# Kernel optimization log

Hardware: AMD Instinct MI355X
Metric: run time of the kernel (lower is better)

## Reference

```python
import jax, jax.numpy as jnp
import numpy as np

EPS = 1e-05
IN_FEATURES = 1024
OUT_FEATURES = 512
M = 65536


def setup_inputs() -> dict:
    key = jax.random.key(0)
    k_x, k_w, k_b = jax.random.split(key, 3)
    x = jax.random.normal(k_x, (M, IN_FEATURES), dtype=jnp.float32)
    # kaiming_uniform(a=sqrt(5)) on [out, in]: bound = sqrt(6/((1+a^2)*fan_in)) = 1/sqrt(fan_in)
    bound = 1.0 / np.sqrt(IN_FEATURES)
    weight = jax.random.uniform(k_w, (OUT_FEATURES, IN_FEATURES), dtype=jnp.float32,
                                minval=-bound, maxval=bound)
    bias = jax.random.uniform(k_b, (OUT_FEATURES,), dtype=jnp.float32,
                              minval=-bound, maxval=bound)
    gamma = jnp.ones((OUT_FEATURES,), dtype=jnp.float32)
    beta = jnp.zeros((OUT_FEATURES,), dtype=jnp.float32)
    scale = jnp.ones((1,), dtype=jnp.float32)
    return {"x": x, "weight": weight, "bias": bias,
            "gamma": gamma, "beta": beta, "scale": scale}


def reference(x, weight, bias, gamma, beta, scale):
    # GEMM + bias: [M, N]
    acc = jnp.einsum('mk,nk->mn', x, weight) + bias[None, :]
    # Row-wise normalization over N (as the fused kernel computes per row)
    mean = jnp.mean(acc, axis=1, keepdims=True)
    var = jnp.mean((acc - mean) ** 2, axis=1, keepdims=True)
    normalized = (acc - mean) / jnp.sqrt(var + EPS)
    scaled = (normalized * gamma[None, :] + beta[None, :]) * scale[0]
    # Row softmax over N
    return jax.nn.softmax(scaled, axis=1)
```

## Files before the change

### kernel.cpp

```cpp
#include <hip/hip_runtime.h>
#include <hip/hip_bf16.h>

constexpr int KD = 1024;
constexpr int ND = 512;
constexpr int NT = 16;
constexpr float EPSV = 1e-5f;

using f32x4  = __attribute__((ext_vector_type(4))) float;
using bf16x8 = __attribute__((ext_vector_type(8))) short;
using u16x8  = __attribute__((ext_vector_type(8))) unsigned short;

__device__ __forceinline__ unsigned short f2bf(float f) {
  unsigned int u = __builtin_bit_cast(unsigned int, f);
  return (unsigned short)((u + 0x7fffu + ((u >> 16) & 1u)) >> 16);
}

__device__ __forceinline__ u16x8 pack8(float4 a, float4 b) {
  u16x8 v;
  v[0] = f2bf(a.x); v[1] = f2bf(a.y); v[2] = f2bf(a.z); v[3] = f2bf(a.w);
  v[4] = f2bf(b.x); v[5] = f2bf(b.y); v[6] = f2bf(b.z); v[7] = f2bf(b.w);
  return v;
}

__device__ __forceinline__ unsigned short cvt1(float f) {
  __hip_bfloat16 h = __float2bfloat16(f);
  return __builtin_bit_cast(unsigned short, h);
}

__device__ __forceinline__ float bf2f(unsigned short s) {
  unsigned int u = (unsigned int)s << 16;
  return __builtin_bit_cast(float, u);
}

__device__ __forceinline__ void gload16(const void* g, void* l) {
  __builtin_amdgcn_global_load_lds(
      (const __attribute__((address_space(1))) void*)g,
      (__attribute__((address_space(3))) void*)l, 16, 0, 0);
}

#define WAITV8()  asm volatile("s_waitcnt vmcnt(8)" ::: "memory")
#define WAITV0()  asm volatile("s_waitcnt vmcnt(0)" ::: "memory")
#define LGKM0()   do { asm volatile("s_waitcnt lgkmcnt(0)" ::: "memory"); \
                       __builtin_amdgcn_sched_barrier(0); } while (0)
#define SCHEDB()  __builtin_amdgcn_sched_barrier(0)

__global__ void wconvert_kernel(const float* __restrict__ w,
                                unsigned short* __restrict__ wb) {
  int i = (blockIdx.x * blockDim.x + threadIdx.x) * 8;
  float4 a = *reinterpret_cast<const float4*>(w + i);
  float4 b = *reinterpret_cast<const float4*>(w + i + 4);
  *reinterpret_cast<u16x8*>(wb + i) = pack8(a, b);
}

__global__ __launch_bounds__(512, 2)
void fused_kernel(const float* __restrict__ x,
                  const unsigned short* __restrict__ wb,
                  const float* __restrict__ bias,
                  const float* __restrict__ gamma,
                  const float* __restrict__ beta,
                  const float* __restrict__ scalep,
                  float* __restrict__ out) {
  __shared__ unsigned short As[2][128 * 64];
  __shared__ unsigned short Bs[2][512 * 64];

  const int tid  = threadIdx.x;
  const int lane = tid & 63;
  const int wid  = tid >> 6;
  const int wr   = wid >> 2;
  const int wcq  = wid & 3;
  const int l15  = lane & 15;
  const int lg   = lane >> 4;

  const long bm  = (long)blockIdx.x * 128;

  f32x4 acc[4][8] = {};

  const int arow0 = wid * 16 + lg;
  const float* asrc = x + (bm + arow0) * KD + l15 * 4;
  int aw[4];
  #pragma unroll
  for (int q = 0; q < 4; ++q) {
    int row = arow0 + q * 4;
    aw[q] = row * 128 + (((l15 >> 1) ^ (row & 7)) * 16) + ((l15 & 1) * 8);
  }

  int bsrc[8];
  #pragma unroll
  for (int p = 0; p < 8; ++p) {
    int n = p * 64 + (tid >> 3);
    int u = (tid & 7) ^ (n & 7);
    bsrc[p] = n * KD + u * 8;
  }

  int ard[4], brd[8];
  #pragma unroll
  for (int i = 0; i < 4; ++i) {
    int row = wr * 64 + i * 16 + l15;
    ard[i] = row * 128 + (lg ^ (row & 7)) * 16;
  }
  #pragma unroll
  for (int i = 0; i < 8; ++i) {
    int n = wcq * 128 + i * 16 + l15;
    brd[i] = n * 128 + (lg ^ (n & 7)) * 16;
  }

#define ISSUE_A(t) do { \
    qa0 = *reinterpret_cast<const float4*>(asrc + (t) * 64 + 0 * 4 * KD); \
    qa1 = *reinterpret_cast<const float4*>(asrc + (t) * 64 + 1 * 4 * KD); \
    qa2 = *reinterpret_cast<const float4*>(asrc + (t) * 64 + 2 * 4 * KD); \
    qa3 = *reinterpret_cast<const float4*>(asrc + (t) * 64 + 3 * 4 * KD); } while (0)

#define ISSUE_B(t, bufi) do { \
    gload16(wb + bsrc[0] + (t) * 64, (char*)Bs[bufi] + 0 * 8192 + tid * 16); \
    gload16(wb + bsrc[1] + (t) * 64, (char*)Bs[bufi] + 1 * 8192 + tid * 16); \
    gload16(wb + bsrc[2] + (t) * 64, (char*)Bs[bufi] + 2 * 8192 + tid * 16); \
    gload16(wb + bsrc[3] + (t) * 64, (char*)Bs[bufi] + 3 * 8192 + tid * 16); \
    gload16(wb + bsrc[4] + (t) * 64, (char*)Bs[bufi] + 4 * 8192 + tid * 16); \
    gload16(wb + bsrc[5] + (t) * 64, (char*)Bs[bufi] + 5 * 8192 + tid * 16); \
    gload16(wb + bsrc[6] + (t) * 64, (char*)Bs[bufi] + 6 * 8192 + tid * 16); \
    gload16(wb + bsrc[7] + (t) * 64, (char*)Bs[bufi] + 7 * 8192 + tid * 16); } while (0)

#define WA1(qr, qi, bufi) do { \
    union { unsigned short s[4]; unsigned long long v; } c_; \
    c_.s[0] = cvt1(qr.x); c_.s[1] = cvt1(qr.y); \
    c_.s[2] = cvt1(qr.z); c_.s[3] = cvt1(qr.w); \
    *reinterpret_cast<unsigned long long*>((char*)As[bufi] + aw[qi]) = c_.v; } while (0)

#define WRITE_A(bufi) do { const int wb_ = (bufi); \
    WA1(qa0, 0, wb_); WA1(qa1, 1, wb_); WA1(qa2, 2, wb_); WA1(qa3, 3, wb_); } while (0)

#define PHASE(ks, bufc) do { \
    const char* ab_ = (const char*)As[bufc]; \
    const char* bb_ = (const char*)Bs[bufc]; \
    const int kx_ = (ks) * 64; \
    bf16x8 b0_ = *reinterpret_cast<const bf16x8*>(bb_ + (brd[0] ^ kx_)); \
    bf16x8 b1_ = *reinterpret_cast<const bf16x8*>(bb_ + (brd[1] ^ kx_)); \
    bf16x8 b2_ = *reinterpret_cast<const bf16x8*>(bb_ + (brd[2] ^ kx_)); \
    bf16x8 b3_ = *reinterpret_cast<const bf16x8*>(bb_ + (brd[3] ^ kx_)); \
    bf16x8 b4_ = *reinterpret_cast<const bf16x8*>(bb_ + (brd[4] ^ kx_)); \
    bf16x8 b5_ = *reinterpret_cast<const bf16x8*>(bb_ + (brd[5] ^ kx_)); \
    bf16x8 b6_ = *reinterpret_cast<const bf16x8*>(bb_ + (brd[6] ^ kx_)); \
    bf16x8 b7_ = *reinterpret_cast<const bf16x8*>(bb_ + (brd[7] ^ kx_)); \
    bf16x8 a0_ = *reinterpret_cast<const bf16x8*>(ab_ + (ard[0] ^ kx_)); \
    bf16x8 a1_ = *reinterpret_cast<const bf16x8*>(ab_ + (ard[1] ^ kx_)); \
    bf16x8 a2_ = *reinterpret_cast<const bf16x8*>(ab_ + (ard[2] ^ kx_)); \
    bf16x8 a3_ = *reinterpret_cast<const bf16x8*>(ab_ + (ard[3] ^ kx_)); \
    LGKM0(); \
    __builtin_amdgcn_s_setprio(1); \
    acc[0][0] = __builtin_amdgcn_mfma_f32_16x16x32_bf16(a0_, b0_, acc[0][0], 0, 0, 0); \
    acc[0][1] = __builtin_amdgcn_mfma_f32_16x16x32_bf16(a0_, b1_, acc[0][1], 0, 0, 0); \
    acc[0][2] = __builtin_amdgcn_mfma_f32_16x16x32_bf16(a0_, b2_, acc[0][2], 0, 0, 0); \
    acc[0][3] = __builtin_amdgcn_mfma_f32_16x16x32_bf16(a0_, b3_, acc[0][3], 0, 0, 0); \
    acc[0][4] = __builtin_amdgcn_mfma_f32_16x16x32_bf16(a0_, b4_, acc[0][4], 0, 0, 0); \
    acc[0][5] = __builtin_amdgcn_mfma_f32_16x16x32_bf16(a0_, b5_, acc[0][5], 0, 0, 0); \
    acc[0][6] = __builtin_amdgcn_mfma_f32_16x16x32_bf16(a0_, b6_, acc[0][6], 0, 0, 0); \
    acc[0][7] = __builtin_amdgcn_mfma_f32_16x16x32_bf16(a0_, b7_, acc[0][7], 0, 0, 0); \
    acc[1][0] = __builtin_amdgcn_mfma_f32_16x16x32_bf16(a1_, b0_, acc[1][0], 0, 0, 0); \
    acc[1][1] = __builtin_amdgcn_mfma_f32_16x16x32_bf16(a1_, b1_, acc[1][1], 0, 0, 0); \
    acc[1][2] = __builtin_amdgcn_mfma_f32_16x16x32_bf16(a1_, b2_, acc[1][2], 0, 0, 0); \
    acc[1][3] = __builtin_amdgcn_mfma_f32_16x16x32_bf16(a1_, b3_, acc[1][3], 0, 0, 0); \
    acc[1][4] = __builtin_amdgcn_mfma_f32_16x16x32_bf16(a1_, b4_, acc[1][4], 0, 0, 0); \
    acc[1][5] = __builtin_amdgcn_mfma_f32_16x16x32_bf16(a1_, b5_, acc[1][5], 0, 0, 0); \
    acc[1][6] = __builtin_amdgcn_mfma_f32_16x16x32_bf16(a1_, b6_, acc[1][6], 0, 0, 0); \
    acc[1][7] = __builtin_amdgcn_mfma_f32_16x16x32_bf16(a1_, b7_, acc[1][7], 0, 0, 0); \
    acc[2][0] = __builtin_amdgcn_mfma_f32_16x16x32_bf16(a2_, b0_, acc[2][0], 0, 0, 0); \
    acc[2][1] = __builtin_amdgcn_mfma_f32_16x16x32_bf16(a2_, b1_, acc[2][1], 0, 0, 0); \
    acc[2][2] = __builtin_amdgcn_mfma_f32_16x16x32_bf16(a2_, b2_, acc[2][2], 0, 0, 0); \
    acc[2][3] = __builtin_amdgcn_mfma_f32_16x16x32_bf16(a2_, b3_, acc[2][3], 0, 0, 0); \
    acc[2][4] = __builtin_amdgcn_mfma_f32_16x16x32_bf16(a2_, b4_, acc[2][4], 0, 0, 0); \
    acc[2][5] = __builtin_amdgcn_mfma_f32_16x16x32_bf16(a2_, b5_, acc[2][5], 0, 0, 0); \
    acc[2][6] = __builtin_amdgcn_mfma_f32_16x16x32_bf16(a2_, b6_, acc[2][6], 0, 0, 0); \
    acc[2][7] = __builtin_amdgcn_mfma_f32_16x16x32_bf16(a2_, b7_, acc[2][7], 0, 0, 0); \
    acc[3][0] = __builtin_amdgcn_mfma_f32_16x16x32_bf16(a3_, b0_, acc[3][0], 0, 0, 0); \
    acc[3][1] = __builtin_amdgcn_mfma_f32_16x16x32_bf16(a3_, b1_, acc[3][1], 0, 0, 0); \
    acc[3][2] = __builtin_amdgcn_mfma_f32_16x16x32_bf16(a3_, b2_, acc[3][2], 0, 0, 0); \
    acc[3][3] = __builtin_amdgcn_mfma_f32_16x16x32_bf16(a3_, b3_, acc[3][3], 0, 0, 0); \
    acc[3][4] = __builtin_amdgcn_mfma_f32_16x16x32_bf16(a3_, b4_, acc[3][4], 0, 0, 0); \
    acc[3][5] = __builtin_amdgcn_mfma_f32_16x16x32_bf16(a3_, b5_, acc[3][5], 0, 0, 0); \
    acc[3][6] = __builtin_amdgcn_mfma_f32_16x16x32_bf16(a3_, b6_, acc[3][6], 0, 0, 0); \
    acc[3][7] = __builtin_amdgcn_mfma_f32_16x16x32_bf16(a3_, b7_, acc[3][7], 0, 0, 0); \
    __builtin_amdgcn_s_setprio(0); \
    SCHEDB(); } while (0)

  float4 qa0, qa1, qa2, qa3;

  ISSUE_A(0);    SCHEDB();
  ISSUE_B(0, 0); SCHEDB();
  WAITV8();
  WRITE_A(0);
  WAITV0();
  LGKM0();
  __builtin_amdgcn_s_barrier();
  SCHEDB();

  for (int t = 0; t < NT; ++t) {
    const int cur = t & 1;
    const int tp  = (t + 1 < NT) ? t + 1 : NT - 1;
    ISSUE_A(tp);          SCHEDB();
    PHASE(0, cur);
    ISSUE_B(tp, cur ^ 1); SCHEDB();
    PHASE(1, cur);
    WAITV8();
    WRITE_A(cur ^ 1);
    WAITV0();
    LGKM0();
    __builtin_amdgcn_s_barrier();
    SCHEDB();
  }

  float* redS = (float*)As[0];
  float* redQ = redS + 640;
  float* rowA = redQ + 640;
  float* rowB = rowA + 128;

  const int col0 = wcq * 128 + l15;
  const float sc = scalep[0];
  float bs8[8], gs8[8], bb8[8];
  #pragma unroll
  for (int ni = 0; ni < 8; ++ni) {
    bs8[ni] = bias[col0 + ni * 16];
    gs8[ni] = gamma[col0 + ni * 16] * sc;
    bb8[ni] = beta[col0 + ni * 16] * sc;
  }

  #pragma unroll
  for (int mi = 0; mi < 4; ++mi) {
    #pragma unroll
    for (int j = 0; j < 4; ++j) {
      float s = 0.f, q = 0.f;
      #pragma unroll
      for (int ni = 0; ni < 8; ++ni) {
        float v = acc[mi][ni][j] + bs8[ni];
        acc[mi][ni][j] = v;
        s += v;
        q = fmaf(v, v, q);
      }
      #pragma unroll
      for (int m = 1; m < 16; m <<= 1) {
        s += __shfl_xor(s, m, 64);
        q += __shfl_xor(q, m, 64);
      }
      if (l15 == 0) {
        int r = wr * 64 + mi * 16 + lg * 4 + j;
        redS[r * 5 + wcq] = s;
        redQ[r * 5 + wcq] = q;
      }
    }
  }
  __syncthreads();
  if (tid < 128) {
    float s = redS[tid * 5 + 0] + redS[tid * 5 + 1] + redS[tid * 5 + 2] + redS[tid * 5 + 3];
    float q = redQ[tid * 5 + 0] + redQ[tid * 5 + 1] + redQ[tid * 5 + 2] + redQ[tid * 5 + 3];
    float mu = s * (1.f / ND);
    rowA[tid] = mu;
    rowB[tid] = rsqrtf(q * (1.f / ND) - mu * mu + EPSV);
  }
  __syncthreads();

  #pragma unroll
  for (int mi = 0; mi < 4; ++mi) {
    #pragma unroll
    for (int j = 0; j < 4; ++j) {
      int r = wr * 64 + mi * 16 + lg * 4 + j;
      float mu = rowA[r], rs = rowB[r];
      float pm = -3.402823466e38f;
      #pragma unroll
      for (int ni = 0; ni < 8; ++ni) {
        float v = (acc[mi][ni][j] - mu) * rs;
        v = fmaf(v, gs8[ni], bb8[ni]);
        acc[mi][ni][j] = v;
        pm = fmaxf(pm, v);
      }
      #pragma unroll
      for (int m = 1; m < 16; m <<= 1) pm = fmaxf(pm, __shfl_xor(pm, m, 64));
      if (l15 == 0) redS[r * 5 + wcq] = pm;
    }
  }
  __syncthreads();
  if (tid < 128) {
    rowA[tid] = fmaxf(fmaxf(redS[tid * 5 + 0], redS[tid * 5 + 1]),
                      fmaxf(redS[tid * 5 + 2], redS[tid * 5 + 3]));
  }
  __syncthreads();

  #pragma unroll
  for (int mi = 0; mi < 4; ++mi) {
    #pragma unroll
    for (int j = 0; j < 4; ++j) {
      int r = wr * 64 + mi * 16 + lg * 4 + j;
      float rmx = rowA[r];
      float ps = 0.f;
      #pragma unroll
      for (int ni = 0; ni < 8; ++ni) {
        float e = __expf(acc[mi][ni][j] - rmx);
        acc[mi][ni][j] = e;
        ps += e;
      }
      #pragma unroll
      for (int m = 1; m < 16; m <<= 1) ps += __shfl_xor(ps, m, 64);
      if (l15 == 0) redQ[r * 5 + wcq] = ps;
    }
  }
  __syncthreads();
  if (tid < 128) {
    rowB[tid] = 1.f / (redQ[tid * 5 + 0] + redQ[tid * 5 + 1] +
                       redQ[tid * 5 + 2] + redQ[tid * 5 + 3]);
  }
  __syncthreads();

  #pragma unroll
  for (int mi = 0; mi < 4; ++mi) {
    #pragma unroll
    for (int j = 0; j < 4; ++j) {
      int r = wr * 64 + mi * 16 + lg * 4 + j;
      float rd = rowB[r];
      float* op = out + (bm + r) * ND + col0;
      #pragma unroll
      for (int ni = 0; ni < 8; ++ni)
        __builtin_nontemporal_store(acc[mi][ni][j] * rd, op + ni * 16);
    }
  }
#undef ISSUE_A
#undef ISSUE_B
#undef WA1
#undef WRITE_A
#undef PHASE
}

__global__ void fused_fallback(const float* __restrict__ x,
                               const float* __restrict__ wf,
                               const float* __restrict__ bias,
                               const float* __restrict__ gamma,
                               const float* __restrict__ beta,
                               const float* __restrict__ scalep,
                               float* __restrict__ out) {
  long row = blockIdx.x;
  int t = threadIdx.x;
  float s = 0.f;
  const float* xr = x + row * KD;
  const float* wr_ = wf + (size_t)t * KD;
  for (int k = 0; k < KD; ++k) s += xr[k] * wr_[k];
  s += bias[t];
  __shared__ float buf[ND];
  buf[t] = s;
  __syncthreads();
  __shared__ float red[2];
  if (t == 0) {
    float sum = 0.f, sq = 0.f;
    for (int i = 0; i < ND; ++i) { sum += buf[i]; sq += buf[i] * buf[i]; }
    float mu = sum / ND;
    red[0] = mu;
    red[1] = rsqrtf(sq / ND - mu * mu + EPSV);
  }
  __syncthreads();
  float zv = (s - red[0]) * red[1] * gamma[t] * scalep[0] + beta[t] * scalep[0];
  buf[t] = zv;
  __syncthreads();
  __shared__ float red2[2];
  if (t == 0) {
    float mxv = -3.4e38f;
    for (int i = 0; i < ND; ++i) mxv = fmaxf(mxv, buf[i]);
    float den = 0.f;
    for (int i = 0; i < ND; ++i) den += __expf(buf[i] - mxv);
    red2[0] = mxv; red2[1] = 1.f / den;
  }
  __syncthreads();
  out[row * ND + t] = __expf(zv - red2[0]) * red2[1];
}

extern "C" void kernel_launch(void* const* d_in, const int* in_sizes, int n_in,
                              void* d_out, int out_size, void* d_ws, size_t ws_size,
                              hipStream_t stream) {
  const float* x     = (const float*)d_in[0];
  const float* w     = (const float*)d_in[1];
  const float* bias  = (const float*)d_in[2];
  const float* gamma = (const float*)d_in[3];
  const float* beta  = (const float*)d_in[4];
  const float* scale = (const float*)d_in[5];
  float* out = (float*)d_out;

  const int Mrows = in_sizes[0] / KD;
  const size_t wb_bytes = (size_t)ND * KD * sizeof(unsigned short);

  if (ws_size >= wb_bytes) {
    unsigned short* wbuf = (unsigned short*)d_ws;
    wconvert_kernel<<<(ND * KD) / (256 * 8), 256, 0, stream>>>(w, wbuf);
    fused_kernel<<<Mrows / 128, 512, 0, stream>>>(x, wbuf, bias, gamma, beta,
                                                  scale, out);
  } else {
    fused_fallback<<<Mrows, ND, 0, stream>>>(x, w, bias, gamma, beta, scale, out);
  }
}
```

Measured before the change: 140.5 us.

## Use 1024-thread blocks with 64-column wave tiles and earlier B prefetch

Doubles the block to 16 waves, each computing a 64x64 tile instead of 64x128, halving accumulator registers per thread and splitting A/B global loads across more threads. The B tile prefetch for the next k-step is issued before the first MFMA phase instead of between phases. Row reductions for layernorm and softmax now combine 8 per-wave partials. This adds more LDS fragment reads overall and a larger block that may limit scheduling flexibility.

Result: no change. 139.1 us (-0.9%).

```diff
diff --git a/kernel.cpp b/kernel.cpp
--- a/kernel.cpp
+++ b/kernel.cpp
@@ -27,18 +27,13 @@
   return __builtin_bit_cast(unsigned short, h);
 }
 
-__device__ __forceinline__ float bf2f(unsigned short s) {
-  unsigned int u = (unsigned int)s << 16;
-  return __builtin_bit_cast(float, u);
-}
-
 __device__ __forceinline__ void gload16(const void* g, void* l) {
   __builtin_amdgcn_global_load_lds(
       (const __attribute__((address_space(1))) void*)g,
       (__attribute__((address_space(3))) void*)l, 16, 0, 0);
 }
 
-#define WAITV8()  asm volatile("s_waitcnt vmcnt(8)" ::: "memory")
+#define WAITV4()  asm volatile("s_waitcnt vmcnt(4)" ::: "memory")
 #define WAITV0()  asm volatile("s_waitcnt vmcnt(0)" ::: "memory")
 #define LGKM0()   do { asm volatile("s_waitcnt lgkmcnt(0)" ::: "memory"); \
                        __builtin_amdgcn_sched_barrier(0); } while (0)
@@ -52,7 +47,7 @@
   *reinterpret_cast<u16x8*>(wb + i) = pack8(a, b);
 }
 
-__global__ __launch_bounds__(512, 2)
+__global__ __launch_bounds__(1024, 4)
 void fused_kernel(const float* __restrict__ x,
                   const unsigned short* __restrict__ wb,
                   const float* __restrict__ bias,
@@ -66,59 +61,53 @@
   const int tid  = threadIdx.x;
   const int lane = tid & 63;
   const int wid  = tid >> 6;
-  const int wr   = wid >> 2;
-  const int wcq  = wid & 3;
+  const int wr   = wid >> 3;
+  const int wcn  = wid & 7;
   const int l15  = lane & 15;
   const int lg   = lane >> 4;
 
   const long bm  = (long)blockIdx.x * 128;
 
-  f32x4 acc[4][8] = {};
-
-  const int arow0 = wid * 16 + lg;
+  f32x4 acc[4][4] = {};
+
+  const int arow0 = wid * 8 + lg;
   const float* asrc = x + (bm + arow0) * KD + l15 * 4;
-  int aw[4];
-  #pragma unroll
-  for (int q = 0; q < 4; ++q) {
+  int aw[2];
+  #pragma unroll
+  for (int q = 0; q < 2; ++q) {
     int row = arow0 + q * 4;
     aw[q] = row * 128 + (((l15 >> 1) ^ (row & 7)) * 16) + ((l15 & 1) * 8);
   }
 
-  int bsrc[8];
-  #pragma unroll
-  for (int p = 0; p < 8; ++p) {
-    int n = p * 64 + (tid >> 3);
+  int bsrc[4];
+  #pragma unroll
+  for (int p = 0; p < 4; ++p) {
+    int n = p * 128 + (tid >> 3);
     int u = (tid & 7) ^ (n & 7);
     bsrc[p] = n * KD + u * 8;
   }
 
-  int ard[4], brd[8];
+  int ard[4], brd[4];
   #pragma unroll
   for (int i = 0; i < 4; ++i) {
     int row = wr * 64 + i * 16 + l15;
     ard[i] = row * 128 + (lg ^ (row & 7)) * 16;
   }
   #pragma unroll
-  for (int i = 0; i < 8; ++i) {
-    int n = wcq * 128 + i * 16 + l15;
+  for (int i = 0; i < 4; ++i) {
+    int n = wcn * 64 + i * 16 + l15;
     brd[i] = n * 128 + (lg ^ (n & 7)) * 16;
   }
 
 #define ISSUE_A(t) do { \
     qa0 = *reinterpret_cast<const float4*>(asrc + (t) * 64 + 0 * 4 * KD); \
-    qa1 = *reinterpret_cast<const float4*>(asrc + (t) * 64 + 1 * 4 * KD); \
-    qa2 = *reinterpret_cast<const float4*>(asrc + (t) * 64 + 2 * 4 * KD); \
-    qa3 = *reinterpret_cast<const float4*>(asrc + (t) * 64 + 3 * 4 * KD); } while (0)
+    qa1 = *reinterpret_cast<const float4*>(asrc + (t) * 64 + 1 * 4 * KD); } while (0)
 
 #define ISSUE_B(t, bufi) do { \
-    gload16(wb + bsrc[0] + (t) * 64, (char*)Bs[bufi] + 0 * 8192 + tid * 16); \
-    gload16(wb + bsrc[1] + (t) * 64, (char*)Bs[bufi] + 1 * 8192 + tid * 16); \
-    gload16(wb + bsrc[2] + (t) * 64, (char*)Bs[bufi] + 2 * 8192 + tid * 16); \
-    gload16(wb + bsrc[3] + (t) * 64, (char*)Bs[bufi] + 3 * 8192 + tid * 16); \
-    gload16(wb + bsrc[4] + (t) * 64, (char*)Bs[bufi] + 4 * 8192 + tid * 16); \
-    gload16(wb + bsrc[5] + (t) * 64, (char*)Bs[bufi] + 5 * 8192 + tid * 16); \
-    gload16(wb + bsrc[6] + (t) * 64, (char*)Bs[bufi] + 6 * 8192 + tid * 16); \
-    gload16(wb + bsrc[7] + (t) * 64, (char*)Bs[bufi] + 7 * 8192 + tid * 16); } while (0)
+    gload16(wb + bsrc[0] + (t) * 64, (char*)Bs[bufi] + 0 * 16384 + tid * 16); \
+    gload16(wb + bsrc[1] + (t) * 64, (char*)Bs[bufi] + 1 * 16384 + tid * 16); \
+    gload16(wb + bsrc[2] + (t) * 64, (char*)Bs[bufi] + 2 * 16384 + tid * 16); \
+    gload16(wb + bsrc[3] + (t) * 64, (char*)Bs[bufi] + 3 * 16384 + tid * 16); } while (0)
 
 #define WA1(qr, qi, bufi) do { \
     union { unsigned short s[4]; unsigned long long v; } c_; \
@@ -127,7 +116,7 @@
     *reinterpret_cast<unsigned long long*>((char*)As[bufi] + aw[qi]) = c_.v; } while (0)
 
 #define WRITE_A(bufi) do { const int wb_ = (bufi); \
-    WA1(qa0, 0, wb_); WA1(qa1, 1, wb_); WA1(qa2, 2, wb_); WA1(qa3, 3, wb_); } while (0)
+    WA1(qa0, 0, wb_); WA1(qa1, 1, wb_); } while (0)
 
 #define PHASE(ks, bufc) do { \
     const char* ab_ = (const char*)As[bufc]; \
@@ -137,10 +126,6 @@
     bf16x8 b1_ = *reinterpret_cast<const bf16x8*>(bb_ + (brd[1] ^ kx_)); \
     bf16x8 b2_ = *reinterpret_cast<const bf16x8*>(bb_ + (brd[2] ^ kx_)); \
     bf16x8 b3_ = *reinterpret_cast<const bf16x8*>(bb_ + (brd[3] ^ kx_)); \
-    bf16x8 b4_ = *reinterpret_cast<const bf16x8*>(bb_ + (brd[4] ^ kx_)); \
-    bf16x8 b5_ = *reinterpret_cast<const bf16x8*>(bb_ + (brd[5] ^ kx_)); \
-    bf16x8 b6_ = *reinterpret_cast<const bf16x8*>(bb_ + (brd[6] ^ kx_)); \
-    bf16x8 b7_ = *reinterpret_cast<const bf16x8*>(bb_ + (brd[7] ^ kx_)); \
     bf16x8 a0_ = *reinterpret_cast<const bf16x8*>(ab_ + (ard[0] ^ kx_)); \
     bf16x8 a1_ = *reinterpret_cast<const bf16x8*>(ab_ + (ard[1] ^ kx_)); \
     bf16x8 a2_ = *reinterpret_cast<const bf16x8*>(ab_ + (ard[2] ^ kx_)); \
@@ -151,42 +136,26 @@
     acc[0][1] = __builtin_amdgcn_mfma_f32_16x16x32_bf16(a0_, b1_, acc[0][1], 0, 0, 0); \
     acc[0][2] = __builtin_amdgcn_mfma_f32_16x16x32_bf16(a0_, b2_, acc[0][2], 0, 0, 0); \
     acc[0][3] = __builtin_amdgcn_mfma_f32_16x16x32_bf16(a0_, b3_, acc[0][3], 0, 0, 0); \
-    acc[0][4] = __builtin_amdgcn_mfma_f32_16x16x32_bf16(a0_, b4_, acc[0][4], 0, 0, 0); \
-    acc[0][5] = __builtin_amdgcn_mfma_f32_16x16x32_bf16(a0_, b5_, acc[0][5], 0, 0, 0); \
-    acc[0][6] = __builtin_amdgcn_mfma_f32_16x16x32_bf16(a0_, b6_, acc[0][6], 0, 0, 0); \
-    acc[0][7] = __builtin_amdgcn_mfma_f32_16x16x32_bf16(a0_, b7_, acc[0][7], 0, 0, 0); \
     acc[1][0] = __builtin_amdgcn_mfma_f32_16x16x32_bf16(a1_, b0_, acc[1][0], 0, 0, 0); \
     acc[1][1] = __builtin_amdgcn_mfma_f32_16x16x32_bf16(a1_, b1_, acc[1][1], 0, 0, 0); \
     acc[1][2] = __builtin_amdgcn_mfma_f32_16x16x32_bf16(a1_, b2_, acc[1][2], 0, 0, 0); \
     acc[1][3] = __builtin_amdgcn_mfma_f32_16x16x32_bf16(a1_, b3_, acc[1][3], 0, 0, 0); \
-    acc[1][4] = __builtin_amdgcn_mfma_f32_16x16x32_bf16(a1_, b4_, acc[1][4], 0, 0, 0); \
-    acc[1][5] = __builtin_amdgcn_mfma_f32_16x16x32_bf16(a1_, b5_, acc[1][5], 0, 0, 0); \
-    acc[1][6] = __builtin_amdgcn_mfma_f32_16x16x32_bf16(a1_, b6_, acc[1][6], 0, 0, 0); \
-    acc[1][7] = __builtin_amdgcn_mfma_f32_16x16x32_bf16(a1_, b7_, acc[1][7], 0, 0, 0); \
     acc[2][0] = __builtin_amdgcn_mfma_f32_16x16x32_bf16(a2_, b0_, acc[2][0], 0, 0, 0); \
     acc[2][1] = __builtin_amdgcn_mfma_f32_16x16x32_bf16(a2_, b1_, acc[2][1], 0, 0, 0); \
     acc[2][2] = __builtin_amdgcn_mfma_f32_16x16x32_bf16(a2_, b2_, acc[2][2], 0, 0, 0); \
     acc[2][3] = __builtin_amdgcn_mfma_f32_16x16x32_bf16(a2_, b3_, acc[2][3], 0, 0, 0); \
-    acc[2][4] = __builtin_amdgcn_mfma_f32_16x16x32_bf16(a2_, b4_, acc[2][4], 0, 0, 0); \
-    acc[2][5] = __builtin_amdgcn_mfma_f32_16x16x32_bf16(a2_, b5_, acc[2][5], 0, 0, 0); \
-    acc[2][6] = __builtin_amdgcn_mfma_f32_16x16x32_bf16(a2_, b6_, acc[2][6], 0, 0, 0); \
-    acc[2][7] = __builtin_amdgcn_mfma_f32_16x16x32_bf16(a2_, b7_, acc[2][7], 0, 0, 0); \
     acc[3][0] = __builtin_amdgcn_mfma_f32_16x16x32_bf16(a3_, b0_, acc[3][0], 0, 0, 0); \
     acc[3][1] = __builtin_amdgcn_mfma_f32_16x16x32_bf16(a3_, b1_, acc[3][1], 0, 0, 0); \
     acc[3][2] = __builtin_amdgcn_mfma_f32_16x16x32_bf16(a3_, b2_, acc[3][2], 0, 0, 0); \
     acc[3][3] = __builtin_amdgcn_mfma_f32_16x16x32_bf16(a3_, b3_, acc[3][3], 0, 0, 0); \
-    acc[3][4] = __builtin_amdgcn_mfma_f32_16x16x32_bf16(a3_, b4_, acc[3][4], 0, 0, 0); \
-    acc[3][5] = __builtin_amdgcn_mfma_f32_16x16x32_bf16(a3_, b5_, acc[3][5], 0, 0, 0); \
-    acc[3][6] = __builtin_amdgcn_mfma_f32_16x16x32_bf16(a3_, b6_, acc[3][6], 0, 0, 0); \
-    acc[3][7] = __builtin_amdgcn_mfma_f32_16x16x32_bf16(a3_, b7_, acc[3][7], 0, 0, 0); \
     __builtin_amdgcn_s_setprio(0); \
     SCHEDB(); } while (0)
 
-  float4 qa0, qa1, qa2, qa3;
+  float4 qa0, qa1;
 
   ISSUE_A(0);    SCHEDB();
   ISSUE_B(0, 0); SCHEDB();
-  WAITV8();
+  WAITV4();
   WRITE_A(0);
   WAITV0();
   LGKM0();
@@ -197,10 +166,10 @@
     const int cur = t & 1;
     const int tp  = (t + 1 < NT) ? t + 1 : NT - 1;
     ISSUE_A(tp);          SCHEDB();
+    ISSUE_B(tp, cur ^ 1); SCHEDB();
     PHASE(0, cur);
-    ISSUE_B(tp, cur ^ 1); SCHEDB();
     PHASE(1, cur);
-    WAITV8();
+    WAITV4();
     WRITE_A(cur ^ 1);
     WAITV0();
     LGKM0();
@@ -209,18 +178,18 @@
   }
 
   float* redS = (float*)As[0];
-  float* redQ = redS + 640;
-  float* rowA = redQ + 640;
+  float* redQ = redS + 1152;
+  float* rowA = redQ + 1152;
   float* rowB = rowA + 128;
 
-  const int col0 = wcq * 128 + l15;
+  const int col0 = wcn * 64 + l15;
   const float sc = scalep[0];
-  float bs8[8], gs8[8], bb8[8];
-  #pragma unroll
-  for (int ni = 0; ni < 8; ++ni) {
-    bs8[ni] = bias[col0 + ni * 16];
-    gs8[ni] = gamma[col0 + ni * 16] * sc;
-    bb8[ni] = beta[col0 + ni * 16] * sc;
+  float bs4[4], gs4[4], bb4[4];
+  #pragma unroll
+  for (int ni = 0; ni < 4; ++ni) {
+    bs4[ni] = bias[col0 + ni * 16];
+    gs4[ni] = gamma[col0 + ni * 16] * sc;
+    bb4[ni] = beta[col0 + ni * 16] * sc;
   }
 
   #pragma unroll
@@ -229,8 +198,8 @@
     for (int j = 0; j < 4; ++j) {
       float s = 0.f, q = 0.f;
       #pragma unroll
-      for (int ni = 0; ni < 8; ++ni) {
-        float v = acc[mi][ni][j] + bs8[ni];
+      for (int ni = 0; ni < 4; ++ni) {
+        float v = acc[mi][ni][j] + bs4[ni];
         acc[mi][ni][j] = v;
         s += v;
         q = fmaf(v, v, q);
@@ -242,15 +211,16 @@
       }
       if (l15 == 0) {
         int r = wr * 64 + mi * 16 + lg * 4 + j;
-        redS[r * 5 + wcq] = s;
-        redQ[r * 5 + wcq] = q;
+        redS[r * 9 + wcn] = s;
+        redQ[r * 9 + wcn] = q;
       }
     }
   }
   __syncthreads();
   if (tid < 128) {
-    float s = redS[tid * 5 + 0] + redS[tid * 5 + 1] + redS[tid * 5 + 2] + redS[tid * 5 + 3];
-    float q = redQ[tid * 5 + 0] + redQ[tid * 5 + 1] + redQ[tid * 5 + 2] + redQ[tid * 5 + 3];
+    float s = 0.f, q = 0.f;
+    #pragma unroll
+    for (int k = 0; k < 8; ++k) { s += redS[tid * 9 + k]; q += redQ[tid * 9 + k]; }
     float mu = s * (1.f / ND);
     rowA[tid] = mu;
     rowB[tid] = rsqrtf(q * (1.f / ND) - mu * mu + EPSV);
@@ -265,21 +235,24 @@
       float mu = rowA[r], rs = rowB[r];
       float pm = -3.402823466e38f;
       #pragma unroll
-      for (int ni = 0; ni < 8; ++ni) {
+      for (int ni = 0; ni < 4; ++ni) {
         float v = (acc[mi][ni][j] - mu) * rs;
-        v = fmaf(v, gs8[ni], bb8[ni]);
+        v = fmaf(v, gs4[ni], bb4[ni]);
         acc[mi][ni][j] = v;
         pm = fmaxf(pm, v);
       }
       #pragma unroll
       for (int m = 1; m < 16; m <<= 1) pm = fmaxf(pm, __shfl_xor(pm, m, 64));
-      if (l15 == 0) redS[r * 5 + wcq] = pm;
+      if (l15 == 0) redS[r * 9 + wcn] = pm;
     }
   }
   __syncthreads();
   if (tid < 128) {
-    rowA[tid] = fmaxf(fmaxf(redS[tid * 5 + 0], redS[tid * 5 + 1]),
-                      fmaxf(redS[tid * 5 + 2], redS[tid * 5 + 3]));
+    float m0 = fmaxf(fmaxf(redS[tid * 9 + 0], redS[tid * 9 + 1]),
+                     fmaxf(redS[tid * 9 + 2], redS[tid * 9 + 3]));
+    float m1 = fmaxf(fmaxf(redS[tid * 9 + 4], redS[tid * 9 + 5]),
+                     fmaxf(redS[tid * 9 + 6], redS[tid * 9 + 7]));
+    rowA[tid] = fmaxf(m0, m1);
   }
   __syncthreads();
 
@@ -291,20 +264,22 @@
       float rmx = rowA[r];
       float ps = 0.f;
       #pragma unroll
-      for (int ni = 0; ni < 8; ++ni) {
+      for (int ni = 0; ni < 4; ++ni) {
         float e = __expf(acc[mi][ni][j] - rmx);
         acc[mi][ni][j] = e;
         ps += e;
       }
       #pragma unroll
       for (int m = 1; m < 16; m <<= 1) ps += __shfl_xor(ps, m, 64);
-      if (l15 == 0) redQ[r * 5 + wcq] = ps;
+      if (l15 == 0) redQ[r * 9 + wcn] = ps;
     }
   }
   __syncthreads();
   if (tid < 128) {
-    rowB[tid] = 1.f / (redQ[tid * 5 + 0] + redQ[tid * 5 + 1] +
-                       redQ[tid * 5 + 2] + redQ[tid * 5 + 3]);
+    float s = 0.f;
+    #pragma unroll
+    for (int k = 0; k < 8; ++k) s += redQ[tid * 9 + k];
+    rowB[tid] = 1.f / s;
   }
   __syncthreads();
 
@@ -316,7 +291,7 @@
       float rd = rowB[r];
       float* op = out + (bm + r) * ND + col0;
       #pragma unroll
-      for (int ni = 0; ni < 8; ++ni)
+      for (int ni = 0; ni < 4; ++ni)
         __builtin_nontemporal_store(acc[mi][ni][j] * rd, op + ni * 16);
     }
   }
@@ -385,8 +360,8 @@
   if (ws_size >= wb_bytes) {
     unsigned short* wbuf = (unsigned short*)d_ws;
     wconvert_kernel<<<(ND * KD) / (256 * 8), 256, 0, stream>>>(w, wbuf);
-    fused_kernel<<<Mrows / 128, 512, 0, stream>>>(x, wbuf, bias, gamma, beta,
-                                                  scale, out);
+    fused_kernel<<<Mrows / 128, 1024, 0, stream>>>(x, wbuf, bias, gamma, beta,
+                                                   scale, out);
   } else {
     fused_fallback<<<Mrows, ND, 0, stream>>>(x, w, bias, gamma, beta, scale, out);
   }
```
